# Performance work log

Measured on AMD Instinct MI355X. Metric: run time of the kernel, lower is better.

Reference implementation:

```python
import jax, jax.numpy as jnp
import numpy as np

N = 100000   # nodes
E = 1600000  # edges
IN, H, C = 128, 128, 40


def setup_inputs() -> dict:
    key = jax.random.key(0)
    ks = jax.random.split(key, 8)
    feat = jax.random.normal(ks[0], (N, IN), jnp.float32)
    src = jax.random.randint(ks[1], (E,), 0, N, jnp.int32)
    dst = jax.random.randint(ks[2], (E,), 0, N, jnp.int32)
    # Glorot-ish init like dgl GraphConv.reset_parameters
    W0 = jax.random.normal(ks[3], (IN, H), jnp.float32) * (1.0 / np.sqrt(IN))
    W1 = jax.random.normal(ks[4], (H, H), jnp.float32) * (1.0 / np.sqrt(H))
    W2 = jax.random.normal(ks[5], (H, C), jnp.float32) * (1.0 / np.sqrt(H))
    b0 = jnp.zeros((H,), jnp.float32)
    b1 = jnp.zeros((H,), jnp.float32)
    b2 = jnp.zeros((C,), jnp.float32)
    return {"feat": feat, "src": src, "dst": dst,
            "W0": W0, "b0": b0, "W1": W1, "b1": b1, "W2": W2, "b2": b2}


def _graph_conv(h, src, dst, W, b):
    # dgl GraphConv with norm='both': D_out^{-1/2} pre-scale, sum-aggregate,
    # D_in^{-1/2} post-scale; degrees clamped to min 1. Weight applied before
    # aggregation (in_feats >= out_feats path) -- math is identical either way.
    ones = jnp.ones((src.shape[0],), h.dtype)
    deg_out = jnp.maximum(jax.ops.segment_sum(ones, src, num_segments=N), 1.0)
    deg_in = jnp.maximum(jax.ops.segment_sum(ones, dst, num_segments=N), 1.0)
    h = h * (deg_out ** -0.5)[:, None]
    h = h @ W                                   # [N, out]
    agg = jax.ops.segment_sum(h[src], dst, num_segments=N)  # gather+scatter
    return agg * (deg_in ** -0.5)[:, None] + b


def reference(feat, src, dst, W0, b0, W1, b1, W2, b2):
    h = jax.nn.relu(_graph_conv(feat, src, dst, W0, b0))  # dropout p=0 -> identity
    h = jax.nn.relu(_graph_conv(h, src, dst, W1, b1))
    return _graph_conv(h, src, dst, W2, b2)
```

## Files before the change

kernel.cpp:

```cpp
#include <hip/hip_runtime.h>

#define NN 100000
#define EE 1600000
#define ELLW 64
#define GEMMN ((NN + 31) / 32)
#define BQ ((EE / 4 + 511) / 512)
#define GRID_BG (BQ * 5)

#define NBKT 196
#define BSH 9
#define CAPD 10240
#define CAPS 10240

typedef int iv4 __attribute__((ext_vector_type(4)));

__device__ __forceinline__ unsigned int pack_bf2(float a, float b) {
    unsigned int ua = __float_as_uint(a);
    ua += 0x7FFFu + ((ua >> 16) & 1u);
    unsigned int ub = __float_as_uint(b);
    ub += 0x7FFFu + ((ub >> 16) & 1u);
    return (ua >> 16) | (ub & 0xFFFF0000u);
}

__device__ __forceinline__ void gemm128_body(const float* __restrict__ X,
                                             const float* __restrict__ W, unsigned int* __restrict__ Y,
                                             int row0, int tid, float* Xs) {
    const float4* X4 = (const float4*)X;
#pragma unroll
    for (int idx = tid; idx < 1024; idx += 256) {
        int r = idx & 31, c4 = idx >> 5;
        int row = row0 + r;
        float4 v = X4[(size_t)row * 32 + c4];
        Xs[(c4 * 4 + 0) * 32 + r] = v.x;
        Xs[(c4 * 4 + 1) * 32 + r] = v.y;
        Xs[(c4 * 4 + 2) * 32 + r] = v.z;
        Xs[(c4 * 4 + 3) * 32 + r] = v.w;
    }
    __syncthreads();
    int cg = tid & 31;
    int rg = tid >> 5;
    float a[4][4];
#pragma unroll
    for (int r = 0; r < 4; ++r)
#pragma unroll
        for (int c = 0; c < 4; ++c) a[r][c] = 0.f;
    const float4* W4 = (const float4*)W;
#pragma unroll 4
    for (int k = 0; k < 128; ++k) {
        float4 xv = *(const float4*)&Xs[k * 32 + rg * 4];
        float4 wv = W4[k * 32 + cg];
        float xr[4] = {xv.x, xv.y, xv.z, xv.w};
        float wc[4] = {wv.x, wv.y, wv.z, wv.w};
#pragma unroll
        for (int r = 0; r < 4; ++r)
#pragma unroll
            for (int c = 0; c < 4; ++c) a[r][c] = fmaf(xr[r], wc[c], a[r][c]);
    }
    int rbase = row0 + rg * 4;
    uint2* Y2 = (uint2*)Y;
#pragma unroll
    for (int r = 0; r < 4; ++r) {
        Y2[(size_t)(rbase + r) * 32 + cg] =
            make_uint2(pack_bf2(a[r][0], a[r][1]), pack_bf2(a[r][2], a[r][3]));
    }
}

__global__ __launch_bounds__(256) void k_buildA_gemm0(const int* __restrict__ src, const int* __restrict__ dst,
                                                      int* __restrict__ curD, int* __restrict__ curS,
                                                      unsigned int* __restrict__ stagD,
                                                      unsigned short* __restrict__ stagS,
                                                      const float* __restrict__ X, const float* __restrict__ W,
                                                      unsigned int* __restrict__ Y) {
    __shared__ float Xs[128 * 32];
    int tid = threadIdx.x;
    int q = blockIdx.x / 5, rem = blockIdx.x % 5;
    if (rem) {
        int g = q * 4 + (rem - 1);
        if (g < GEMMN) gemm128_body(X, W, Y, g * 32, tid, Xs);
        return;
    }
    int* sh = (int*)Xs;
    for (int i = tid; i < 1536; i += 256) sh[i] = 0;
    __syncthreads();

    const iv4* s4p = (const iv4*)src;
    const iv4* d4p = (const iv4*)dst;
    const int n4 = EE / 4;
    iv4 sv[2], dv[2];
    int have[2];
#pragma unroll
    for (int h = 0; h < 2; ++h) {
        int i4 = q * 512 + h * 256 + tid;
        have[h] = (i4 < n4);
        if (have[h]) {
            sv[h] = __builtin_nontemporal_load(&s4p[i4]);
            dv[h] = __builtin_nontemporal_load(&d4p[i4]);
        }
    }
#pragma unroll
    for (int h = 0; h < 2; ++h) {
        if (have[h]) {
            int ss[4] = {sv[h].x, sv[h].y, sv[h].z, sv[h].w};
            int dd[4] = {dv[h].x, dv[h].y, dv[h].z, dv[h].w};
#pragma unroll
            for (int k = 0; k < 4; ++k) {
                atomicAdd(&sh[dd[k] >> BSH], 1);
                atomicAdd(&sh[256 + (ss[k] >> BSH)], 1);
            }
        }
    }
    __syncthreads();
    if (tid < NBKT) {
        int hd = sh[tid];
        sh[512 + tid] = hd ? atomicAdd(&curD[tid], hd) : 0;
        int hs = sh[256 + tid];
        sh[768 + tid] = hs ? atomicAdd(&curS[tid], hs) : 0;
    }
    __syncthreads();
#pragma unroll
    for (int h = 0; h < 2; ++h) {
        if (have[h]) {
            int ss[4] = {sv[h].x, sv[h].y, sv[h].z, sv[h].w};
            int dd[4] = {dv[h].x, dv[h].y, dv[h].z, dv[h].w};
#pragma unroll
            for (int k = 0; k < 4; ++k) {
                int bd = dd[k] >> BSH;
                int od = atomicAdd(&sh[1024 + bd], 1);
                stagD[(size_t)bd * CAPD + sh[512 + bd] + od] =
                    ((unsigned int)ss[k] << BSH) | (unsigned int)(dd[k] & 511);
                int bs = ss[k] >> BSH;
                int os = atomicAdd(&sh[1280 + bs], 1);
                stagS[(size_t)bs * CAPS + sh[768 + bs] + os] = (unsigned short)(ss[k] & 511);
            }
        }
    }
}

__global__ __launch_bounds__(256) void k_buildB(const int* __restrict__ curD, const int* __restrict__ curS,
                                                const unsigned int* __restrict__ stagD,
                                                const unsigned short* __restrict__ stagS,
                                                int* __restrict__ din, int* __restrict__ dout,
                                                int* __restrict__ ell) {
    __shared__ int cl[512];
    int tid = threadIdx.x;
    int b = blockIdx.x;
    for (int i = tid; i < 512; i += 256) cl[i] = 0;
    __syncthreads();
    if (b < NBKT) {
        int n0 = b << BSH;
        int cnt = min(curD[b], CAPD);
        const unsigned int* sg = stagD + (size_t)b * CAPD;
        for (int i = tid; i < cnt; i += 256) {
            unsigned int v = sg[i];
            int dlow = (int)(v & 511u);
            int s = (int)(v >> BSH);
            int p = atomicAdd(&cl[dlow], 1);
            if (p < ELLW) ell[(size_t)(n0 + dlow) * ELLW + p] = s;
        }
        __syncthreads();
        for (int i = tid; i < 512; i += 256) {
            int node = n0 + i;
            if (node < NN) din[node] = cl[i];
        }
    } else {
        int bs = b - NBKT;
        int n0 = bs << BSH;
        int cnt = min(curS[bs], CAPS);
        const unsigned short* sg = stagS + (size_t)bs * CAPS;
        for (int i = tid; i < cnt; i += 256) {
            atomicAdd(&cl[sg[i]], 1);
        }
        __syncthreads();
        for (int i = tid; i < 512; i += 256) {
            int node = n0 + i;
            if (node < NN) dout[node] = cl[i];
        }
    }
}

__global__ __launch_bounds__(256) void k_gathergemm128(const unsigned int* __restrict__ h,
                                                       const int* __restrict__ din, const int* __restrict__ dout,
                                                       const int* __restrict__ ell,
                                                       const float* __restrict__ bias,
                                                       const float* __restrict__ W,
                                                       unsigned int* __restrict__ Y, int so_mode) {
    __shared__ float Xs[128 * 36];
    int tid = threadIdx.x;
    int wv = tid >> 6, lane = tid & 63;
    int row0 = blockIdx.x * 32;
    float2 bb = ((const float2*)bias)[lane];
    for (int j8 = 0; j8 < 8; ++j8) {
        int r = wv * 8 + j8;
        int v = row0 + r;
        int dv = din[v];
        int cnt = min(dv, ELLW);
        int cl = ell[(size_t)v * ELLW + lane];
        int cls = (lane < cnt) ? cl : 0;
        float scl = 1.f;
        if (so_mode) scl = rsqrtf((float)max(1, dout[cls]));
        float sx = 0.f, sy = 0.f;
        for (int j = 0; j < cnt; j += 8) {
            int cc[8]; float mk[8]; unsigned int t[8];
#pragma unroll
            for (int k = 0; k < 8; ++k) {
                int jj = j + k;
                int jc = jj < cnt ? jj : cnt - 1;
                cc[k] = __shfl(cls, jc);
                float sw = so_mode ? __shfl(scl, jc) : 1.f;
                mk[k] = (jj < cnt) ? sw : 0.f;
            }
#pragma unroll
            for (int k = 0; k < 8; ++k) t[k] = h[(size_t)cc[k] * 64 + lane];
#pragma unroll
            for (int k = 0; k < 8; ++k) {
                float x = __uint_as_float(t[k] << 16);
                float y = __uint_as_float(t[k] & 0xFFFF0000u);
                sx = fmaf(mk[k], x, sx);
                sy = fmaf(mk[k], y, sy);
            }
        }
        float si = rsqrtf((float)max(1, dv));
        float so = rsqrtf((float)max(1, dout[v]));
        float ox = fmaxf(sx * si + bb.x, 0.f) * so;
        float oy = fmaxf(sy * si + bb.y, 0.f) * so;
        Xs[(2 * lane) * 36 + r] = ox;
        Xs[(2 * lane + 1) * 36 + r] = oy;
    }
    __syncthreads();
    int cg = tid & 31, rg = tid >> 5;
    float a[4][4];
#pragma unroll
    for (int r = 0; r < 4; ++r)
#pragma unroll
        for (int c = 0; c < 4; ++c) a[r][c] = 0.f;
    const float4* W4 = (const float4*)W;
#pragma unroll 4
    for (int k = 0; k < 128; ++k) {
        float4 xv = *(const float4*)&Xs[k * 36 + rg * 4];
        float4 wv4 = W4[k * 32 + cg];
        float xr[4] = {xv.x, xv.y, xv.z, xv.w};
        float wc[4] = {wv4.x, wv4.y, wv4.z, wv4.w};
#pragma unroll
        for (int r = 0; r < 4; ++r)
#pragma unroll
            for (int c = 0; c < 4; ++c) a[r][c] = fmaf(xr[r], wc[c], a[r][c]);
    }
    int rbase = row0 + rg * 4;
    uint2* Y2 = (uint2*)Y;
#pragma unroll
    for (int r = 0; r < 4; ++r) {
        Y2[(size_t)(rbase + r) * 32 + cg] =
            make_uint2(pack_bf2(a[r][0], a[r][1]), pack_bf2(a[r][2], a[r][3]));
    }
}

__global__ __launch_bounds__(256) void k_gathergemm40(const unsigned int* __restrict__ h,
                                                      const int* __restrict__ din, const int* __restrict__ dout,
                                                      const int* __restrict__ ell,
                                                      const float* __restrict__ bias,
                                                      const float* __restrict__ W,
                                                      unsigned int* __restrict__ Y) {
    __shared__ float Xs[128 * 36];
    __shared__ float Os[32 * 40];
    int tid = threadIdx.x;
    int wv = tid >> 6, lane = tid & 63;
    int row0 = blockIdx.x * 32;
    float2 bb = ((const float2*)bias)[lane];
    for (int j8 = 0; j8 < 8; ++j8) {
        int r = wv * 8 + j8;
        int v = row0 + r;
        int dv = din[v];
        int cnt = min(dv, ELLW);
        int cl = ell[(size_t)v * ELLW + lane];
        int cls = (lane < cnt) ? cl : 0;
        float sx = 0.f, sy = 0.f;
        for (int j = 0; j < cnt; j += 8) {
            int cc[8]; float mk[8]; unsigned int t[8];
#pragma unroll
            for (int k = 0; k < 8; ++k) {
                int jj = j + k;
                cc[k] = __shfl(cls, jj < cnt ? jj : cnt - 1);
                mk[k] = (jj < cnt) ? 1.f : 0.f;
            }
#pragma unroll
            for (int k = 0; k < 8; ++k) t[k] = h[(size_t)cc[k] * 64 + lane];
#pragma unroll
            for (int k = 0; k < 8; ++k) {
                float x = __uint_as_float(t[k] << 16);
                float y = __uint_as_float(t[k] & 0xFFFF0000u);
                sx = fmaf(mk[k], x, sx);
                sy = fmaf(mk[k], y, sy);
            }
        }
        float si = rsqrtf((float)max(1, dv));
        float so = rsqrtf((float)max(1, dout[v]));
        float ox = fmaxf(sx * si + bb.x, 0.f) * so;
        float oy = fmaxf(sy * si + bb.y, 0.f) * so;
        Xs[(2 * lane) * 36 + r] = ox;
        Xs[(2 * lane + 1) * 36 + r] = oy;
    }
    __syncthreads();
    int rg = tid >> 3;
    int cg = tid & 7;
    float a[5] = {0.f, 0.f, 0.f, 0.f, 0.f};
    for (int k = 0; k < 128; ++k) {
        float x = Xs[k * 36 + rg];
#pragma unroll
        for (int c = 0; c < 5; ++c) a[c] = fmaf(x, W[k * 40 + cg * 5 + c], a[c]);
    }
#pragma unroll
    for (int c = 0; c < 5; ++c) Os[rg * 40 + cg * 5 + c] = a[c];
    __syncthreads();
    for (int i = tid; i < 640; i += 256) {
        int row = i / 20, pj = i % 20;
        Y[(size_t)(row0 + row) * 32 + pj] = pack_bf2(Os[row * 40 + 2 * pj], Os[row * 40 + 2 * pj + 1]);
    }
}

__global__ __launch_bounds__(256) void k_gather40(const unsigned short* __restrict__ h, const int* __restrict__ din,
                                                  const int* __restrict__ ell,
                                                  const float* __restrict__ b, float* __restrict__ out, int n) {
    int wv = threadIdx.x >> 6, lane = threadIdx.x & 63;
    int v = blockIdx.x * 4 + wv;
    if (v >= n) return;
    int dv = din[v];
    int cnt = min(dv, ELLW);
    int cl = ell[(size_t)v * ELLW + lane];
    int cls = (lane < cnt) ? cl : 0;
    float s = 0.f;
    for (int j = 0; j < cnt; j += 8) {
        int cc[8]; float mk[8]; unsigned short t[8];
#pragma unroll
        for (int k = 0; k < 8; ++k) {
            int jj = j + k;
            cc[k] = __shfl(cls, jj < cnt ? jj : cnt - 1);
            mk[k] = (jj < cnt) ? 1.f : 0.f;
        }
        if (lane < 40) {
#pragma unroll
            for (int k = 0; k < 8; ++k) t[k] = h[(size_t)cc[k] * 64 + lane];
#pragma unroll
            for (int k = 0; k < 8; ++k)
                s = fmaf(mk[k], __uint_as_float((unsigned int)t[k] << 16), s);
        }
    }
    if (lane < 40) {
        out[(size_t)v * 40 + lane] = s * rsqrtf((float)max(1, dv)) + b[lane];
    }
}

extern "C" void kernel_launch(void* const* d_in, const int* in_sizes, int n_in,
                              void* d_out, int out_size, void* d_ws, size_t ws_size,
                              hipStream_t stream) {
    const float* feat = (const float*)d_in[0];
    const int*   src  = (const int*)d_in[1];
    const int*   dst  = (const int*)d_in[2];
    const float* W0   = (const float*)d_in[3];
    const float* b0   = (const float*)d_in[4];
    const float* W1   = (const float*)d_in[5];
    const float* b1   = (const float*)d_in[6];
    const float* W2   = (const float*)d_in[7];
    const float* b2   = (const float*)d_in[8];
    float* out = (float*)d_out;

    char* w = (char*)d_ws;
    int*   din       = (int*)w;    w += (size_t)NN * 4;
    int*   dout      = (int*)w;    w += (size_t)NN * 4;
    int*   curD      = (int*)w;    w += 256 * 4;
    int*   curS      = (int*)w;    w += 256 * 4;
    int*   ell       = (int*)w;    w += (size_t)NN * ELLW * 4;
    unsigned int*   stagD = (unsigned int*)w;   w += (size_t)NBKT * CAPD * 4;
    unsigned short* stagS = (unsigned short*)w; w += (size_t)NBKT * CAPS * 2;
    unsigned int* h2 = (unsigned int*)w; w += (size_t)NN * 128 * 2;
    unsigned int* h2b = (unsigned int*)w; w += (size_t)NN * 128 * 2;
    unsigned int* h40 = (unsigned int*)w; w += (size_t)NN * 32 * 4;

    (void)hipMemsetAsync(d_ws, 0, (size_t)NN * 8 + 2048, stream);

    k_buildA_gemm0<<<GRID_BG, 256, 0, stream>>>(src, dst, curD, curS, stagD, stagS, feat, W0, h2);
    k_buildB<<<NBKT * 2, 256, 0, stream>>>(curD, curS, stagD, stagS, din, dout, ell);
    k_gathergemm128<<<GEMMN, 256, 0, stream>>>(h2, din, dout, ell, b0, W1, h2b, 1);
    k_gathergemm40<<<GEMMN, 256, 0, stream>>>(h2b, din, dout, ell, b1, W2, h40);
    k_gather40<<<(NN + 3) / 4, 256, 0, stream>>>((const unsigned short*)h40, din, ell, b2, out, NN);
}
```

Before: 491.9 us.

## Split wavefronts into half-waves processing two nodes each with wider gather loads

The gather phases of the three aggregation kernels now assign each 32-lane half of a wavefront to its own node. Each lane loads 8 bytes of bf16 features (uint2) instead of 4, or a packed pair in the final layer. The ELL neighbour list is split into two 32-slot halves, and batches stop early via wave-wide any-checks, with the upper half skipped when no node has more than 32 neighbours. The aim is fewer idle lanes and fewer, wider memory transactions per edge. The cost is more divergence when the two nodes' degrees differ, and higher register pressure from the prefetched per-iteration arrays.

```diff
diff --git a/kernel.cpp b/kernel.cpp
--- a/kernel.cpp
+++ b/kernel.cpp
@@ -178,6 +178,30 @@
     }
 }
 
+#define GG_BATCH(CL, SC, JB, CNT, SO) do {                                         \
+    int cc_[8]; float mk_[8]; uint2 t_[8];                                         \
+    _Pragma("unroll")                                                              \
+    for (int k = 0; k < 8; ++k) {                                                  \
+        int slot = (JB) + k;                                                       \
+        int srcl = (hl << 5) | (slot & 31);                                        \
+        cc_[k] = __shfl((CL), srcl);                                               \
+        float sw = (SO) ? __shfl((SC), srcl) : 1.f;                                \
+        mk_[k] = (slot < (CNT)) ? sw : 0.f;                                        \
+    }                                                                              \
+    _Pragma("unroll")                                                              \
+    for (int k = 0; k < 8; ++k) {                                                  \
+        t_[k] = make_uint2(0u, 0u);                                                \
+        if ((JB) + k < (CNT)) t_[k] = h2v[(size_t)cc_[k] * 32 + ln];               \
+    }                                                                              \
+    _Pragma("unroll")                                                              \
+    for (int k = 0; k < 8; ++k) {                                                  \
+        a0 = fmaf(mk_[k], __uint_as_float(t_[k].x << 16), a0);                     \
+        a1 = fmaf(mk_[k], __uint_as_float(t_[k].x & 0xFFFF0000u), a1);             \
+        a2 = fmaf(mk_[k], __uint_as_float(t_[k].y << 16), a2);                     \
+        a3 = fmaf(mk_[k], __uint_as_float(t_[k].y & 0xFFFF0000u), a3);             \
+    }                                                                              \
+} while (0)
+
 __global__ __launch_bounds__(256) void k_gathergemm128(const unsigned int* __restrict__ h,
                                                        const int* __restrict__ din, const int* __restrict__ dout,
                                                        const int* __restrict__ ell,
@@ -187,44 +211,51 @@
     __shared__ float Xs[128 * 36];
     int tid = threadIdx.x;
     int wv = tid >> 6, lane = tid & 63;
+    int hl = lane >> 5, ln = lane & 31;
     int row0 = blockIdx.x * 32;
-    float2 bb = ((const float2*)bias)[lane];
-    for (int j8 = 0; j8 < 8; ++j8) {
-        int r = wv * 8 + j8;
-        int v = row0 + r;
-        int dv = din[v];
-        int cnt = min(dv, ELLW);
-        int cl = ell[(size_t)v * ELLW + lane];
-        int cls = (lane < cnt) ? cl : 0;
-        float scl = 1.f;
-        if (so_mode) scl = rsqrtf((float)max(1, dout[cls]));
-        float sx = 0.f, sy = 0.f;
-        for (int j = 0; j < cnt; j += 8) {
-            int cc[8]; float mk[8]; unsigned int t[8];
-#pragma unroll
-            for (int k = 0; k < 8; ++k) {
-                int jj = j + k;
-                int jc = jj < cnt ? jj : cnt - 1;
-                cc[k] = __shfl(cls, jc);
-                float sw = so_mode ? __shfl(scl, jc) : 1.f;
-                mk[k] = (jj < cnt) ? sw : 0.f;
-            }
-#pragma unroll
-            for (int k = 0; k < 8; ++k) t[k] = h[(size_t)cc[k] * 64 + lane];
-#pragma unroll
-            for (int k = 0; k < 8; ++k) {
-                float x = __uint_as_float(t[k] << 16);
-                float y = __uint_as_float(t[k] & 0xFFFF0000u);
-                sx = fmaf(mk[k], x, sx);
-                sy = fmaf(mk[k], y, sy);
-            }
-        }
-        float si = rsqrtf((float)max(1, dv));
-        float so = rsqrtf((float)max(1, dout[v]));
-        float ox = fmaxf(sx * si + bb.x, 0.f) * so;
-        float oy = fmaxf(sy * si + bb.y, 0.f) * so;
-        Xs[(2 * lane) * 36 + r] = ox;
-        Xs[(2 * lane + 1) * 36 + r] = oy;
+    int nb = row0 + wv * 8 + hl;
+    int dvh[4], dvo[4], cl0[4], cl1[4];
+    float sc0[4], sc1[4];
+#pragma unroll
+    for (int it = 0; it < 4; ++it) {
+        int v = nb + it * 2;
+        dvh[it] = din[v];
+        dvo[it] = dout[v];
+        cl0[it] = ell[(size_t)v * ELLW + ln];
+        cl1[it] = ell[(size_t)v * ELLW + 32 + ln];
+    }
+#pragma unroll
+    for (int it = 0; it < 4; ++it) {
+        int cnt = min(dvh[it], ELLW);
+        int d0 = 1, d1 = 1;
+        if (so_mode && ln < cnt) d0 = dout[cl0[it]];
+        if (so_mode && ln + 32 < cnt) d1 = dout[cl1[it]];
+        sc0[it] = rsqrtf((float)max(1, d0));
+        sc1[it] = rsqrtf((float)max(1, d1));
+    }
+    float4 bb = ((const float4*)bias)[ln];
+    const uint2* h2v = (const uint2*)h;
+#pragma unroll
+    for (int it = 0; it < 4; ++it) {
+        int r = wv * 8 + it * 2 + hl;
+        int cnt = min(dvh[it], ELLW);
+        float a0 = 0.f, a1 = 0.f, a2 = 0.f, a3 = 0.f;
+        for (int jb = 0; jb < 32; jb += 8) {
+            if (!__any(jb < cnt)) break;
+            GG_BATCH(cl0[it], sc0[it], jb, cnt, so_mode);
+        }
+        if (__any(cnt > 32)) {
+            for (int jb = 32; jb < 64; jb += 8) {
+                if (!__any(jb < cnt)) break;
+                GG_BATCH(cl1[it], sc1[it], jb, cnt, so_mode);
+            }
+        }
+        float si = rsqrtf((float)max(1, dvh[it]));
+        float so = rsqrtf((float)max(1, dvo[it]));
+        Xs[(4 * ln + 0) * 36 + r] = fmaxf(a0 * si + bb.x, 0.f) * so;
+        Xs[(4 * ln + 1) * 36 + r] = fmaxf(a1 * si + bb.y, 0.f) * so;
+        Xs[(4 * ln + 2) * 36 + r] = fmaxf(a2 * si + bb.z, 0.f) * so;
+        Xs[(4 * ln + 3) * 36 + r] = fmaxf(a3 * si + bb.w, 0.f) * so;
     }
     __syncthreads();
     int cg = tid & 31, rg = tid >> 5;
@@ -264,40 +295,42 @@
     __shared__ float Os[32 * 40];
     int tid = threadIdx.x;
     int wv = tid >> 6, lane = tid & 63;
+    int hl = lane >> 5, ln = lane & 31;
     int row0 = blockIdx.x * 32;
-    float2 bb = ((const float2*)bias)[lane];
-    for (int j8 = 0; j8 < 8; ++j8) {
-        int r = wv * 8 + j8;
-        int v = row0 + r;
-        int dv = din[v];
-        int cnt = min(dv, ELLW);
-        int cl = ell[(size_t)v * ELLW + lane];
-        int cls = (lane < cnt) ? cl : 0;
-        float sx = 0.f, sy = 0.f;
-        for (int j = 0; j < cnt; j += 8) {
-            int cc[8]; float mk[8]; unsigned int t[8];
-#pragma unroll
-            for (int k = 0; k < 8; ++k) {
-                int jj = j + k;
-                cc[k] = __shfl(cls, jj < cnt ? jj : cnt - 1);
-                mk[k] = (jj < cnt) ? 1.f : 0.f;
-            }
-#pragma unroll
-            for (int k = 0; k < 8; ++k) t[k] = h[(size_t)cc[k] * 64 + lane];
-#pragma unroll
-            for (int k = 0; k < 8; ++k) {
-                float x = __uint_as_float(t[k] << 16);
-                float y = __uint_as_float(t[k] & 0xFFFF0000u);
-                sx = fmaf(mk[k], x, sx);
-                sy = fmaf(mk[k], y, sy);
-            }
-        }
-        float si = rsqrtf((float)max(1, dv));
-        float so = rsqrtf((float)max(1, dout[v]));
-        float ox = fmaxf(sx * si + bb.x, 0.f) * so;
-        float oy = fmaxf(sy * si + bb.y, 0.f) * so;
-        Xs[(2 * lane) * 36 + r] = ox;
-        Xs[(2 * lane + 1) * 36 + r] = oy;
+    int nb = row0 + wv * 8 + hl;
+    int dvh[4], dvo[4], cl0[4], cl1[4];
+#pragma unroll
+    for (int it = 0; it < 4; ++it) {
+        int v = nb + it * 2;
+        dvh[it] = din[v];
+        dvo[it] = dout[v];
+        cl0[it] = ell[(size_t)v * ELLW + ln];
+        cl1[it] = ell[(size_t)v * ELLW + 32 + ln];
+    }
+    float4 bb = ((const float4*)bias)[ln];
+    const uint2* h2v = (const uint2*)h;
+#pragma unroll
+    for (int it = 0; it < 4; ++it) {
+        int r = wv * 8 + it * 2 + hl;
+        int cnt = min(dvh[it], ELLW);
+        float a0 = 0.f, a1 = 0.f, a2 = 0.f, a3 = 0.f;
+        float dummy = 0.f;
+        for (int jb = 0; jb < 32; jb += 8) {
+            if (!__any(jb < cnt)) break;
+            GG_BATCH(cl0[it], dummy, jb, cnt, 0);
+        }
+        if (__any(cnt > 32)) {
+            for (int jb = 32; jb < 64; jb += 8) {
+                if (!__any(jb < cnt)) break;
+                GG_BATCH(cl1[it], dummy, jb, cnt, 0);
+            }
+        }
+        float si = rsqrtf((float)max(1, dvh[it]));
+        float so = rsqrtf((float)max(1, dvo[it]));
+        Xs[(4 * ln + 0) * 36 + r] = fmaxf(a0 * si + bb.x, 0.f) * so;
+        Xs[(4 * ln + 1) * 36 + r] = fmaxf(a1 * si + bb.y, 0.f) * so;
+        Xs[(4 * ln + 2) * 36 + r] = fmaxf(a2 * si + bb.z, 0.f) * so;
+        Xs[(4 * ln + 3) * 36 + r] = fmaxf(a3 * si + bb.w, 0.f) * so;
     }
     __syncthreads();
     int rg = tid >> 3;
@@ -317,35 +350,48 @@
     }
 }
 
-__global__ __launch_bounds__(256) void k_gather40(const unsigned short* __restrict__ h, const int* __restrict__ din,
+__global__ __launch_bounds__(256) void k_gather40(const unsigned int* __restrict__ h, const int* __restrict__ din,
                                                   const int* __restrict__ ell,
                                                   const float* __restrict__ b, float* __restrict__ out, int n) {
-    int wv = threadIdx.x >> 6, lane = threadIdx.x & 63;
-    int v = blockIdx.x * 4 + wv;
-    if (v >= n) return;
+    int tid = threadIdx.x;
+    int wv = tid >> 6, lane = tid & 63;
+    int hl = lane >> 5, ln = lane & 31;
+    int v = blockIdx.x * 8 + wv * 2 + hl;
     int dv = din[v];
     int cnt = min(dv, ELLW);
-    int cl = ell[(size_t)v * ELLW + lane];
-    int cls = (lane < cnt) ? cl : 0;
-    float s = 0.f;
-    for (int j = 0; j < cnt; j += 8) {
-        int cc[8]; float mk[8]; unsigned short t[8];
-#pragma unroll
-        for (int k = 0; k < 8; ++k) {
-            int jj = j + k;
-            cc[k] = __shfl(cls, jj < cnt ? jj : cnt - 1);
-            mk[k] = (jj < cnt) ? 1.f : 0.f;
-        }
-        if (lane < 40) {
-#pragma unroll
-            for (int k = 0; k < 8; ++k) t[k] = h[(size_t)cc[k] * 64 + lane];
-#pragma unroll
-            for (int k = 0; k < 8; ++k)
-                s = fmaf(mk[k], __uint_as_float((unsigned int)t[k] << 16), s);
-        }
-    }
-    if (lane < 40) {
-        out[(size_t)v * 40 + lane] = s * rsqrtf((float)max(1, dv)) + b[lane];
+    int cl0 = ell[(size_t)v * ELLW + ln];
+    int cl1 = ell[(size_t)v * ELLW + 32 + ln];
+    float s0 = 0.f, s1 = 0.f;
+    for (int half = 0; half < 2; ++half) {
+        int clh = half ? cl1 : cl0;
+        int jb0 = half * 32;
+        if (half && !__any(cnt > 32)) break;
+        for (int jb = jb0; jb < jb0 + 32; jb += 8) {
+            if (!__any(jb < cnt)) break;
+            int cc_[8]; float mk_[8]; unsigned int t_[8];
+#pragma unroll
+            for (int k = 0; k < 8; ++k) {
+                int slot = jb + k;
+                int srcl = (hl << 5) | (slot & 31);
+                cc_[k] = __shfl(clh, srcl);
+                mk_[k] = (slot < cnt) ? 1.f : 0.f;
+            }
+#pragma unroll
+            for (int k = 0; k < 8; ++k) {
+                t_[k] = 0u;
+                if (jb + k < cnt) t_[k] = h[(size_t)cc_[k] * 32 + ln];
+            }
+#pragma unroll
+            for (int k = 0; k < 8; ++k) {
+                s0 = fmaf(mk_[k], __uint_as_float(t_[k] << 16), s0);
+                s1 = fmaf(mk_[k], __uint_as_float(t_[k] & 0xFFFF0000u), s1);
+            }
+        }
+    }
+    if (ln < 20) {
+        float si = rsqrtf((float)max(1, dv));
+        float2 bb = ((const float2*)b)[ln];
+        ((float2*)out)[(size_t)v * 20 + ln] = make_float2(s0 * si + bb.x, s1 * si + bb.y);
     }
 }
 
@@ -381,5 +427,5 @@
     k_buildB<<<NBKT * 2, 256, 0, stream>>>(curD, curS, stagD, stagS, din, dout, ell);
     k_gathergemm128<<<GEMMN, 256, 0, stream>>>(h2, din, dout, ell, b0, W1, h2b, 1);
     k_gathergemm40<<<GEMMN, 256, 0, stream>>>(h2b, din, dout, ell, b1, W2, h40);
-    k_gather40<<<(NN + 3) / 4, 256, 0, stream>>>((const unsigned short*)h40, din, ell, b2, out, NN);
-}
+    k_gather40<<<NN / 8, 256, 0, stream>>>(h40, din, ell, b2, out, NN);
+}
```

Result: faster. 480.0 us (-2.4%).
